# Kernel tuning notes

Hardware: AMD Instinct MI355X
Metric: run time of the kernel (lower is better)

The kernel has to match this reference:

```python
import jax, jax.numpy as jnp
import numpy as np

ALPHA, BETA, GAMMA = 1.0, 0.5, 0.3
EPS = 1e-08


def setup_inputs() -> dict:
    key = jax.random.key(0)
    k1, k2, k3, k4, k5 = jax.random.split(key, 5)
    B, C, F = 32, 256, 2048
    return {
        "mag_hat": jax.random.normal(k1, (B, C, F), dtype=jnp.float32),
        "phase_hat": jax.random.normal(k2, (B, C, F), dtype=jnp.float32),
        "mag_target": jax.random.normal(k3, (B, C, F), dtype=jnp.float32),
        "phase_target": jax.random.normal(k4, (B, C, F), dtype=jnp.float32),
        "pci_target": jax.random.uniform(k5, (B, C, C), dtype=jnp.float32),
    }


def _pci(phase):
    # phase: (B, C, F). Naive form is mean_f cos/sin(phi_i - phi_j) over a
    # (B,C,C,F) broadcast; rewrite with cos(a-b)=ca*cb+sa*sb and
    # sin(a-b)=sa*cb-ca*sb as two batched GEMMs on (C,F) matrices.
    c = jnp.cos(phase)
    s = jnp.sin(phase)
    inv_f = 1.0 / phase.shape[-1]
    real = (jnp.einsum('bif,bjf->bij', c, c) + jnp.einsum('bif,bjf->bij', s, s)) * inv_f
    imag = (jnp.einsum('bif,bjf->bij', s, c) - jnp.einsum('bif,bjf->bij', c, s)) * inv_f
    return jnp.sqrt(real * real + imag * imag + EPS)


def reference(mag_hat, phase_hat, mag_target, phase_target, pci_target):
    mag_loss = jnp.mean((mag_hat - mag_target) ** 2)
    phase_loss = jnp.mean(1.0 - jnp.cos(phase_hat - phase_target))
    pci_hat = _pci(phase_hat)
    coh_loss = jnp.mean((pci_hat - pci_target) ** 2)
    total = ALPHA * mag_loss + BETA * phase_loss + GAMMA * coh_loss
    return (total, mag_loss, phase_loss, coh_loss)
```

## Files before the change

kernel.cpp:

```cpp
#include <hip/hip_runtime.h>
#include <hip/hip_bf16.h>

#define ALPHA_ 1.0f
#define BETA_  0.5f
#define GAMMA_ 0.3f
#define EPS_   1e-8f

typedef unsigned short u16;
typedef unsigned int u32;

constexpr int B_ = 32, C_ = 256, F_ = 2048;
constexpr int NTOT = B_ * C_ * F_;
constexpr int G8   = NTOT / 8;
constexpr int NCC  = B_ * C_ * C_;
constexpr int NPOS = 10;
constexpr int KSPL = 4;
constexpr int NBLK = B_ * NPOS * KSPL;
constexpr int NRED = B_ * NPOS * 64 * 64;

__constant__ int TI_[NPOS] = {0, 1, 2, 3, 0, 0, 0, 1, 1, 2};
__constant__ int TJ_[NPOS] = {0, 1, 2, 3, 1, 2, 3, 2, 3, 3};

typedef __bf16 bf16x8 __attribute__((ext_vector_type(8)));
typedef float  f32x4  __attribute__((ext_vector_type(4)));

__device__ __forceinline__ u32 f2bf(float x) {
    unsigned u = __float_as_uint(x);
    u += 0x7fffu + ((u >> 16) & 1u);
    return (u >> 16);
}

__device__ __forceinline__ void async_copy16(const void* g, void* l) {
    __builtin_amdgcn_global_load_lds(
        (const __attribute__((address_space(1))) unsigned int*)g,
        (__attribute__((address_space(3))) unsigned int*)l,
        16, 0, 0);
}

__device__ __forceinline__ void ew_body(int g,
    float4 p0, float4 p1, float4 q0, float4 q1,
    float4 a0, float4 a1, float4 b0, float4 b1,
    float& msum, float& psum, int4* __restrict__ cb4, int4* __restrict__ sb4)
{
    float pv[8] = {p0.x, p0.y, p0.z, p0.w, p1.x, p1.y, p1.z, p1.w};
    float qv[8] = {q0.x, q0.y, q0.z, q0.w, q1.x, q1.y, q1.z, q1.w};
    float av[8] = {a0.x, a0.y, a0.z, a0.w, a1.x, a1.y, a1.z, a1.w};
    float bv[8] = {b0.x, b0.y, b0.z, b0.w, b1.x, b1.y, b1.z, b1.w};
    u32 cu[8], su[8];
    #pragma unroll
    for (int j = 0; j < 8; j++) {
        float dm = av[j] - bv[j];
        msum += dm * dm;
        psum += 1.f - __cosf(pv[j] - qv[j]);
        float s, c;
        __sincosf(pv[j], &s, &c);
        cu[j] = f2bf(c);
        su[j] = f2bf(s);
    }
    cb4[g] = make_int4((int)(cu[0] | (cu[1] << 16)), (int)(cu[2] | (cu[3] << 16)),
                       (int)(cu[4] | (cu[5] << 16)), (int)(cu[6] | (cu[7] << 16)));
    sb4[g] = make_int4((int)(su[0] | (su[1] << 16)), (int)(su[2] | (su[3] << 16)),
                       (int)(su[4] | (su[5] << 16)), (int)(su[6] | (su[7] << 16)));
}

__global__ void __launch_bounds__(256, 4)
ew_kernel(const float4* __restrict__ mh, const float4* __restrict__ ph,
          const float4* __restrict__ mt, const float4* __restrict__ pt,
          int4* __restrict__ cb4, int4* __restrict__ sb4,
          float* __restrict__ accum)
{
    __shared__ float sm[4], sp[4];
    const int tid    = blockIdx.x * 256 + threadIdx.x;
    const int stride = 2048 * 256;
    float msum = 0.f, psum = 0.f;

    #pragma unroll
    for (int half = 0; half < 2; ++half) {
        int g0 = tid + (2 * half) * stride;
        int g1 = g0 + stride;
        float4 p00 = ph[2*g0], p01 = ph[2*g0+1];
        float4 q00 = pt[2*g0], q01 = pt[2*g0+1];
        float4 a00 = mh[2*g0], a01 = mh[2*g0+1];
        float4 b00 = mt[2*g0], b01 = mt[2*g0+1];
        float4 p10 = ph[2*g1], p11 = ph[2*g1+1];
        float4 q10 = pt[2*g1], q11 = pt[2*g1+1];
        float4 a10 = mh[2*g1], a11 = mh[2*g1+1];
        float4 b10 = mt[2*g1], b11 = mt[2*g1+1];
        ew_body(g0, p00, p01, q00, q01, a00, a01, b00, b01, msum, psum, cb4, sb4);
        ew_body(g1, p10, p11, q10, q11, a10, a11, b10, b11, msum, psum, cb4, sb4);
    }

    #pragma unroll
    for (int o = 32; o > 0; o >>= 1) {
        msum += __shfl_down(msum, o, 64);
        psum += __shfl_down(psum, o, 64);
    }
    int lane = threadIdx.x & 63, wv = threadIdx.x >> 6;
    if (lane == 0) { sm[wv] = msum; sp[wv] = psum; }
    __syncthreads();
    if (threadIdx.x == 0) {
        atomicAdd(&accum[0], sm[0] + sm[1] + sm[2] + sm[3]);
        atomicAdd(&accum[1], sp[0] + sp[1] + sp[2] + sp[3]);
    }
}

__global__ void __launch_bounds__(256)
pci_kernel(const u16* __restrict__ cb, const u16* __restrict__ sb,
           float* __restrict__ reb, float* __restrict__ imb)
{
    __shared__ char lds[32768];
    char* la = lds;
    char* lb = lds + 16384;

    const int bid = blockIdx.x;
    const int l   = (bid & 7) * (NBLK / 8) + (bid >> 3);
    const int h   = l & 3;
    const int t4  = l >> 2;
    const int pos = t4 % NPOS;
    const int y   = t4 / NPOS;
    const int i0 = TI_[pos] * 64, j0 = TJ_[pos] * 64;

    const int t    = threadIdx.x;
    const int lane = t & 63, w = t >> 6;
    const int wrow = (w >> 1) * 32, wcol = (w & 1) * 32;
    const int m = lane & 15, q = lane >> 4;

    const char* gA[4];
    const char* gB[4];
    {
        const int p = lane & 15;
        #pragma unroll
        for (int r = 0; r < 4; ++r) {
            int row = w * 16 + r * 4 + (lane >> 4);
            int c   = p ^ (row & 15);
            const u16* arr = (c < 8) ? cb : sb;
            int cc = c & 7;
            gA[r] = (const char*)arr + ((size_t)(y * 256 + i0 + row)) * 4096 + cc * 16 + h * 1024;
            gB[r] = (const char*)arr + ((size_t)(y * 256 + j0 + row)) * 4096 + cc * 16 + h * 1024;
        }
    }

    f32x4 zero = {0.f, 0.f, 0.f, 0.f};
    f32x4 accR[2][2], accSC[2][2], accCS[2][2];
    #pragma unroll
    for (int a = 0; a < 2; a++)
        #pragma unroll
        for (int c = 0; c < 2; c++) {
            accR[a][c] = zero; accSC[a][c] = zero; accCS[a][c] = zero;
        }

    for (int it = 0; it < 8; ++it) {
        __syncthreads();
        #pragma unroll
        for (int r = 0; r < 4; ++r) {
            async_copy16(gA[r], la + w * 4096 + r * 1024);
            async_copy16(gB[r], lb + w * 4096 + r * 1024);
            gA[r] += 128; gB[r] += 128;
        }
        __syncthreads();

        #pragma unroll
        for (int s = 0; s < 2; ++s) {
            bf16x8 fac[2], fas[2], fbc[2], fbs[2];
            #pragma unroll
            for (int a = 0; a < 2; a++) {
                const char* base = la + (wrow + a * 16 + m) * 256;
                int pc = ((4 * s + q) ^ m) * 16;
                fac[a] = *(const bf16x8*)(base + pc);
                fas[a] = *(const bf16x8*)(base + (pc ^ 128));
            }
            #pragma unroll
            for (int c = 0; c < 2; c++) {
                const char* base = lb + (wcol + c * 16 + m) * 256;
                int pc = ((4 * s + q) ^ m) * 16;
                fbc[c] = *(const bf16x8*)(base + pc);
                fbs[c] = *(const bf16x8*)(base + (pc ^ 128));
            }
            #pragma unroll
            for (int a = 0; a < 2; a++)
                #pragma unroll
                for (int c = 0; c < 2; c++) {
                    accR[a][c]  = __builtin_amdgcn_mfma_f32_16x16x32_bf16(fac[a], fbc[c], accR[a][c], 0, 0, 0);
                    accR[a][c]  = __builtin_amdgcn_mfma_f32_16x16x32_bf16(fas[a], fbs[c], accR[a][c], 0, 0, 0);
                    accSC[a][c] = __builtin_amdgcn_mfma_f32_16x16x32_bf16(fas[a], fbc[c], accSC[a][c], 0, 0, 0);
                    accCS[a][c] = __builtin_amdgcn_mfma_f32_16x16x32_bf16(fac[a], fbs[c], accCS[a][c], 0, 0, 0);
                }
        }
    }

    const int tb = (y * NPOS + pos) * 4096;
    #pragma unroll
    for (int a = 0; a < 2; a++)
        #pragma unroll
        for (int c = 0; c < 2; c++) {
            int ii = wrow + a * 16 + q * 4;
            int jj = wcol + c * 16 + m;
            #pragma unroll
            for (int r = 0; r < 4; r++) {
                int idx = tb + (ii + r) * 64 + jj;
                atomicAdd(&reb[idx], accR[a][c][r]);
                atomicAdd(&imb[idx], accSC[a][c][r] - accCS[a][c][r]);
            }
        }
}

__global__ void __launch_bounds__(256)
coh_kernel(const float* __restrict__ reb, const float* __restrict__ imb,
           const float* __restrict__ tgt, float* __restrict__ accum)
{
    __shared__ float sred[4];
    const int tid  = blockIdx.x * 256 + threadIdx.x;
    const int e0   = tid * 8;
    const int tile = e0 >> 12;
    const int y    = tile / NPOS;
    const int pos  = tile % NPOS;
    const int ii   = (e0 & 4095) >> 6;
    const int jj0  = e0 & 63;
    const int ig   = TI_[pos] * 64 + ii;
    const int jg   = TJ_[pos] * 64 + jj0;
    const bool off = (pos >= 4);
    const float invf = 1.0f / (float)F_;
    const float* ty = tgt + (size_t)y * (C_ * C_);
    const float* tr = ty + ig * C_ + jg;

    float4 r0 = *(const float4*)(reb + e0);
    float4 r1 = *(const float4*)(reb + e0 + 4);
    float4 i0 = *(const float4*)(imb + e0);
    float4 i1 = *(const float4*)(imb + e0 + 4);
    float rv[8] = {r0.x, r0.y, r0.z, r0.w, r1.x, r1.y, r1.z, r1.w};
    float iv[8] = {i0.x, i0.y, i0.z, i0.w, i1.x, i1.y, i1.z, i1.w};

    float coh = 0.f;
    #pragma unroll
    for (int j = 0; j < 8; j++) {
        float re = rv[j] * invf, im = iv[j] * invf;
        float p  = sqrtf(re * re + im * im + EPS_);
        float d  = p - tr[j];
        coh += d * d;
        if (off) { float d2 = p - ty[(jg + j) * C_ + ig]; coh += d2 * d2; }
    }

    #pragma unroll
    for (int o = 32; o > 0; o >>= 1) coh += __shfl_down(coh, o, 64);
    int lane = threadIdx.x & 63, w = threadIdx.x >> 6;
    if (lane == 0) sred[w] = coh;
    __syncthreads();
    if (threadIdx.x == 0)
        atomicAdd(&accum[2], sred[0] + sred[1] + sred[2] + sred[3]);
}

__global__ void fin_kernel(const float* __restrict__ accum, float* __restrict__ out)
{
    if (threadIdx.x == 0) {
        float mag = accum[0] * (1.0f / (float)NTOT);
        float phs = accum[1] * (1.0f / (float)NTOT);
        float coh = accum[2] * (1.0f / (float)NCC);
        out[0] = ALPHA_ * mag + BETA_ * phs + GAMMA_ * coh;
        out[1] = mag;
        out[2] = phs;
        out[3] = coh;
    }
}

extern "C" void kernel_launch(void* const* d_in, const int* in_sizes, int n_in,
                              void* d_out, int out_size, void* d_ws, size_t ws_size,
                              hipStream_t stream)
{
    const float* mh  = (const float*)d_in[0];
    const float* ph  = (const float*)d_in[1];
    const float* mt  = (const float*)d_in[2];
    const float* pt  = (const float*)d_in[3];
    const float* tgt = (const float*)d_in[4];
    float* out = (float*)d_out;

    float* accum = (float*)d_ws;
    u16* cb  = (u16*)((char*)d_ws + 256);
    u16* sb  = cb + (size_t)NTOT;
    float* reb = (float*)(sb + (size_t)NTOT);
    float* imb = reb + NRED;

    hipMemsetAsync(d_ws, 0, 16, stream);
    hipMemsetAsync(reb, 0, (size_t)NRED * 2 * sizeof(float), stream);

    ew_kernel<<<2048, 256, 0, stream>>>(
        (const float4*)mh, (const float4*)ph, (const float4*)mt, (const float4*)pt,
        (int4*)cb, (int4*)sb, accum);

    pci_kernel<<<NBLK, 256, 0, stream>>>(cb, sb, reb, imb);

    coh_kernel<<<640, 256, 0, stream>>>(reb, imb, tgt, accum);

    fin_kernel<<<1, 64, 0, stream>>>(accum, out);
}
```

Baseline: 320.9 us.

## Fuse sincos/bf16 conversion into PCI GEMM and replace atomics with per-split slabs

Removes the bf16 cos/sin intermediate arrays. The PCI kernel now reads fp32 phase directly, computes sincos and stores bf16 into swizzled LDS, and skips loading the B tile on diagonal tiles. The K-split partial sums are written to per-split slabs instead of being atomically accumulated, which drops the memset of the accumulation buffer; coh_kernel sums the four slabs. The elementwise kernel is restructured with software-prefetched loads over 8 chunks per thread. The trade-off is that sincos is recomputed in each block that needs a tile, and the explicit fp32 loads replace the async global-to-LDS copies.

```diff
diff --git a/kernel.cpp b/kernel.cpp
--- a/kernel.cpp
+++ b/kernel.cpp
@@ -11,7 +11,6 @@
 
 constexpr int B_ = 32, C_ = 256, F_ = 2048;
 constexpr int NTOT = B_ * C_ * F_;
-constexpr int G8   = NTOT / 8;
 constexpr int NCC  = B_ * C_ * C_;
 constexpr int NPOS = 10;
 constexpr int KSPL = 4;
@@ -30,65 +29,50 @@
     return (u >> 16);
 }
 
-__device__ __forceinline__ void async_copy16(const void* g, void* l) {
-    __builtin_amdgcn_global_load_lds(
-        (const __attribute__((address_space(1))) unsigned int*)g,
-        (__attribute__((address_space(3))) unsigned int*)l,
-        16, 0, 0);
-}
-
-__device__ __forceinline__ void ew_body(int g,
+__device__ __forceinline__ void ew_body(
     float4 p0, float4 p1, float4 q0, float4 q1,
     float4 a0, float4 a1, float4 b0, float4 b1,
-    float& msum, float& psum, int4* __restrict__ cb4, int4* __restrict__ sb4)
+    float& msum, float& psum)
 {
     float pv[8] = {p0.x, p0.y, p0.z, p0.w, p1.x, p1.y, p1.z, p1.w};
     float qv[8] = {q0.x, q0.y, q0.z, q0.w, q1.x, q1.y, q1.z, q1.w};
     float av[8] = {a0.x, a0.y, a0.z, a0.w, a1.x, a1.y, a1.z, a1.w};
     float bv[8] = {b0.x, b0.y, b0.z, b0.w, b1.x, b1.y, b1.z, b1.w};
-    u32 cu[8], su[8];
     #pragma unroll
     for (int j = 0; j < 8; j++) {
         float dm = av[j] - bv[j];
         msum += dm * dm;
         psum += 1.f - __cosf(pv[j] - qv[j]);
-        float s, c;
-        __sincosf(pv[j], &s, &c);
-        cu[j] = f2bf(c);
-        su[j] = f2bf(s);
-    }
-    cb4[g] = make_int4((int)(cu[0] | (cu[1] << 16)), (int)(cu[2] | (cu[3] << 16)),
-                       (int)(cu[4] | (cu[5] << 16)), (int)(cu[6] | (cu[7] << 16)));
-    sb4[g] = make_int4((int)(su[0] | (su[1] << 16)), (int)(su[2] | (su[3] << 16)),
-                       (int)(su[4] | (su[5] << 16)), (int)(su[6] | (su[7] << 16)));
+    }
 }
 
 __global__ void __launch_bounds__(256, 4)
 ew_kernel(const float4* __restrict__ mh, const float4* __restrict__ ph,
           const float4* __restrict__ mt, const float4* __restrict__ pt,
-          int4* __restrict__ cb4, int4* __restrict__ sb4,
           float* __restrict__ accum)
 {
     __shared__ float sm[4], sp[4];
-    const int tid    = blockIdx.x * 256 + threadIdx.x;
-    const int stride = 2048 * 256;
+    const int tid = blockIdx.x * 256 + threadIdx.x;
+    constexpr int STR = 1024 * 256;
     float msum = 0.f, psum = 0.f;
 
-    #pragma unroll
-    for (int half = 0; half < 2; ++half) {
-        int g0 = tid + (2 * half) * stride;
-        int g1 = g0 + stride;
-        float4 p00 = ph[2*g0], p01 = ph[2*g0+1];
-        float4 q00 = pt[2*g0], q01 = pt[2*g0+1];
-        float4 a00 = mh[2*g0], a01 = mh[2*g0+1];
-        float4 b00 = mt[2*g0], b01 = mt[2*g0+1];
-        float4 p10 = ph[2*g1], p11 = ph[2*g1+1];
-        float4 q10 = pt[2*g1], q11 = pt[2*g1+1];
-        float4 a10 = mh[2*g1], a11 = mh[2*g1+1];
-        float4 b10 = mt[2*g1], b11 = mt[2*g1+1];
-        ew_body(g0, p00, p01, q00, q01, a00, a01, b00, b01, msum, psum, cb4, sb4);
-        ew_body(g1, p10, p11, q10, q11, a10, a11, b10, b11, msum, psum, cb4, sb4);
-    }
+    float4 P0[8], P1[8], Q0[8], Q1[8], A0[8], A1[8], B0[8], B1[8];
+
+#define EWLOAD(i) { int g2 = 2 * (tid + (i) * STR);            \
+    P0[i] = ph[g2]; P1[i] = ph[g2 + 1];                         \
+    Q0[i] = pt[g2]; Q1[i] = pt[g2 + 1];                         \
+    A0[i] = mh[g2]; A1[i] = mh[g2 + 1];                         \
+    B0[i] = mt[g2]; B1[i] = mt[g2 + 1]; }
+
+    EWLOAD(0);
+    #pragma unroll
+    for (int i = 0; i < 7; ++i) {
+        EWLOAD(i + 1);
+        __builtin_amdgcn_sched_barrier(0);
+        ew_body(P0[i], P1[i], Q0[i], Q1[i], A0[i], A1[i], B0[i], B1[i], msum, psum);
+    }
+    ew_body(P0[7], P1[7], Q0[7], Q1[7], A0[7], A1[7], B0[7], B1[7], msum, psum);
+#undef EWLOAD
 
     #pragma unroll
     for (int o = 32; o > 0; o >>= 1) {
@@ -104,9 +88,26 @@
     }
 }
 
+__device__ __forceinline__ void stage8(float4 a, float4 b, char* base, int pc) {
+    float v[8] = {a.x, a.y, a.z, a.w, b.x, b.y, b.z, b.w};
+    u32 cu[8], su[8];
+    #pragma unroll
+    for (int j = 0; j < 8; j++) {
+        float s, c;
+        __sincosf(v[j], &s, &c);
+        cu[j] = f2bf(c);
+        su[j] = f2bf(s);
+    }
+    *(int4*)(base + pc) = make_int4(
+        (int)(cu[0] | (cu[1] << 16)), (int)(cu[2] | (cu[3] << 16)),
+        (int)(cu[4] | (cu[5] << 16)), (int)(cu[6] | (cu[7] << 16)));
+    *(int4*)(base + (pc ^ 128)) = make_int4(
+        (int)(su[0] | (su[1] << 16)), (int)(su[2] | (su[3] << 16)),
+        (int)(su[4] | (su[5] << 16)), (int)(su[6] | (su[7] << 16)));
+}
+
 __global__ void __launch_bounds__(256)
-pci_kernel(const u16* __restrict__ cb, const u16* __restrict__ sb,
-           float* __restrict__ reb, float* __restrict__ imb)
+pci_kernel(const float* __restrict__ ph, float* __restrict__ slabs)
 {
     __shared__ char lds[32768];
     char* la = lds;
@@ -119,26 +120,24 @@
     const int pos = t4 % NPOS;
     const int y   = t4 / NPOS;
     const int i0 = TI_[pos] * 64, j0 = TJ_[pos] * 64;
+    const bool diag = (i0 == j0);
+    char* lbp = diag ? la : lb;
 
     const int t    = threadIdx.x;
     const int lane = t & 63, w = t >> 6;
     const int wrow = (w >> 1) * 32, wcol = (w & 1) * 32;
     const int m = lane & 15, q = lane >> 4;
 
-    const char* gA[4];
-    const char* gB[4];
-    {
-        const int p = lane & 15;
-        #pragma unroll
-        for (int r = 0; r < 4; ++r) {
-            int row = w * 16 + r * 4 + (lane >> 4);
-            int c   = p ^ (row & 15);
-            const u16* arr = (c < 8) ? cb : sb;
-            int cc = c & 7;
-            gA[r] = (const char*)arr + ((size_t)(y * 256 + i0 + row)) * 4096 + cc * 16 + h * 1024;
-            gB[r] = (const char*)arr + ((size_t)(y * 256 + j0 + row)) * 4096 + cc * 16 + h * 1024;
-        }
-    }
+    const int row0 = t >> 3, oct = t & 7;
+    const int row1 = row0 + 32;
+    const float* gA0 = ph + ((size_t)(y * 256 + i0 + row0) * 2048 + h * 512 + oct * 8);
+    const float* gA1 = ph + ((size_t)(y * 256 + i0 + row1) * 2048 + h * 512 + oct * 8);
+    const float* gB0 = ph + ((size_t)(y * 256 + j0 + row0) * 2048 + h * 512 + oct * 8);
+    const float* gB1 = ph + ((size_t)(y * 256 + j0 + row1) * 2048 + h * 512 + oct * 8);
+    char* dA0 = la + row0 * 256;  const int pc0 = (oct ^ (row0 & 15)) * 16;
+    char* dA1 = la + row1 * 256;  const int pc1 = (oct ^ (row1 & 15)) * 16;
+    char* dB0 = lb + row0 * 256;
+    char* dB1 = lb + row1 * 256;
 
     f32x4 zero = {0.f, 0.f, 0.f, 0.f};
     f32x4 accR[2][2], accSC[2][2], accCS[2][2];
@@ -151,11 +150,19 @@
 
     for (int it = 0; it < 8; ++it) {
         __syncthreads();
-        #pragma unroll
-        for (int r = 0; r < 4; ++r) {
-            async_copy16(gA[r], la + w * 4096 + r * 1024);
-            async_copy16(gB[r], lb + w * 4096 + r * 1024);
-            gA[r] += 128; gB[r] += 128;
+        float4 a0 = *(const float4*)gA0, a1 = *(const float4*)(gA0 + 4);
+        float4 a2 = *(const float4*)gA1, a3 = *(const float4*)(gA1 + 4);
+        float4 b0, b1, b2, b3;
+        if (!diag) {
+            b0 = *(const float4*)gB0; b1 = *(const float4*)(gB0 + 4);
+            b2 = *(const float4*)gB1; b3 = *(const float4*)(gB1 + 4);
+        }
+        gA0 += 64; gA1 += 64; gB0 += 64; gB1 += 64;
+        stage8(a0, a1, dA0, pc0);
+        stage8(a2, a3, dA1, pc1);
+        if (!diag) {
+            stage8(b0, b1, dB0, pc0);
+            stage8(b2, b3, dB1, pc1);
         }
         __syncthreads();
 
@@ -171,7 +178,7 @@
             }
             #pragma unroll
             for (int c = 0; c < 2; c++) {
-                const char* base = lb + (wcol + c * 16 + m) * 256;
+                const char* base = lbp + (wcol + c * 16 + m) * 256;
                 int pc = ((4 * s + q) ^ m) * 16;
                 fbc[c] = *(const bf16x8*)(base + pc);
                 fbs[c] = *(const bf16x8*)(base + (pc ^ 128));
@@ -188,7 +195,8 @@
         }
     }
 
-    const int tb = (y * NPOS + pos) * 4096;
+    float* sl = slabs + (size_t)h * ((size_t)NRED * 2)
+                      + (size_t)(y * NPOS + pos) * 8192;
     #pragma unroll
     for (int a = 0; a < 2; a++)
         #pragma unroll
@@ -197,16 +205,16 @@
             int jj = wcol + c * 16 + m;
             #pragma unroll
             for (int r = 0; r < 4; r++) {
-                int idx = tb + (ii + r) * 64 + jj;
-                atomicAdd(&reb[idx], accR[a][c][r]);
-                atomicAdd(&imb[idx], accSC[a][c][r] - accCS[a][c][r]);
+                int idx = (ii + r) * 64 + jj;
+                float2 v = make_float2(accR[a][c][r], accSC[a][c][r] - accCS[a][c][r]);
+                *(float2*)(sl + (size_t)idx * 2) = v;
             }
         }
 }
 
 __global__ void __launch_bounds__(256)
-coh_kernel(const float* __restrict__ reb, const float* __restrict__ imb,
-           const float* __restrict__ tgt, float* __restrict__ accum)
+coh_kernel(const float* __restrict__ slabs, const float* __restrict__ tgt,
+           float* __restrict__ accum)
 {
     __shared__ float sred[4];
     const int tid  = blockIdx.x * 256 + threadIdx.x;
@@ -223,12 +231,20 @@
     const float* ty = tgt + (size_t)y * (C_ * C_);
     const float* tr = ty + ig * C_ + jg;
 
-    float4 r0 = *(const float4*)(reb + e0);
-    float4 r1 = *(const float4*)(reb + e0 + 4);
-    float4 i0 = *(const float4*)(imb + e0);
-    float4 i1 = *(const float4*)(imb + e0 + 4);
-    float rv[8] = {r0.x, r0.y, r0.z, r0.w, r1.x, r1.y, r1.z, r1.w};
-    float iv[8] = {i0.x, i0.y, i0.z, i0.w, i1.x, i1.y, i1.z, i1.w};
+    float rv[8] = {0.f, 0.f, 0.f, 0.f, 0.f, 0.f, 0.f, 0.f};
+    float iv[8] = {0.f, 0.f, 0.f, 0.f, 0.f, 0.f, 0.f, 0.f};
+    #pragma unroll
+    for (int hh = 0; hh < 4; hh++) {
+        const float* s = slabs + (size_t)hh * ((size_t)NRED * 2) + (size_t)e0 * 2;
+        float4 v0 = *(const float4*)(s);
+        float4 v1 = *(const float4*)(s + 4);
+        float4 v2 = *(const float4*)(s + 8);
+        float4 v3 = *(const float4*)(s + 12);
+        rv[0] += v0.x; iv[0] += v0.y; rv[1] += v0.z; iv[1] += v0.w;
+        rv[2] += v1.x; iv[2] += v1.y; rv[3] += v1.z; iv[3] += v1.w;
+        rv[4] += v2.x; iv[4] += v2.y; rv[5] += v2.z; iv[5] += v2.w;
+        rv[6] += v3.x; iv[6] += v3.y; rv[7] += v3.z; iv[7] += v3.w;
+    }
 
     float coh = 0.f;
     #pragma unroll
@@ -274,21 +290,17 @@
     float* out = (float*)d_out;
 
     float* accum = (float*)d_ws;
-    u16* cb  = (u16*)((char*)d_ws + 256);
-    u16* sb  = cb + (size_t)NTOT;
-    float* reb = (float*)(sb + (size_t)NTOT);
-    float* imb = reb + NRED;
+    float* slabs = (float*)((char*)d_ws + 256);
 
     hipMemsetAsync(d_ws, 0, 16, stream);
-    hipMemsetAsync(reb, 0, (size_t)NRED * 2 * sizeof(float), stream);
-
-    ew_kernel<<<2048, 256, 0, stream>>>(
+
+    ew_kernel<<<1024, 256, 0, stream>>>(
         (const float4*)mh, (const float4*)ph, (const float4*)mt, (const float4*)pt,
-        (int4*)cb, (int4*)sb, accum);
-
-    pci_kernel<<<NBLK, 256, 0, stream>>>(cb, sb, reb, imb);
-
-    coh_kernel<<<640, 256, 0, stream>>>(reb, imb, tgt, accum);
+        accum);
+
+    pci_kernel<<<NBLK, 256, 0, stream>>>(ph, slabs);
+
+    coh_kernel<<<640, 256, 0, stream>>>(slabs, tgt, accum);
 
     fin_kernel<<<1, 64, 0, stream>>>(accum, out);
 }
```

Result: faster. 308.5 us (-3.9%).
